# Kernel tuning notes

Measured on AMD Instinct MI355X. Metric: run time of the kernel, lower is better.

## Reference

```python
import jax, jax.numpy as jnp
import numpy as np

D_MODEL = 512
N_HEADS = 8
D_HEAD = D_MODEL // N_HEADS
SCALE = D_HEAD ** -0.5


def _rel_shift(x):
    # x: (b, h, qlen, klen) -> Transformer-XL relative shift
    b, h, qlen, klen = x.shape
    x = jnp.pad(x, ((0, 0), (0, 0), (0, 0), (1, 0)))        # (b,h,q,k+1)
    x = x.reshape(b, h, klen + 1, qlen)
    x = x[:, :, 1:, :].reshape(b, h, qlen, klen)
    return x


def setup_inputs() -> dict:
    key = jax.random.key(0)
    ks = jax.random.split(key, 12)
    B, S = 2, 2048
    P = 2 * S - 1
    w = lambda k, shape: (jax.random.normal(k, shape, jnp.float32) * 0.02)
    return {
        "x": jax.random.normal(ks[0], (B, S, D_MODEL), jnp.float32),
        "pos_emb": jax.random.normal(ks[1], (P, D_MODEL), jnp.float32),
        "Wq": w(ks[2], (D_MODEL, D_MODEL)), "bq": jnp.zeros((D_MODEL,), jnp.float32),
        "Wk": w(ks[3], (D_MODEL, D_MODEL)), "bk": jnp.zeros((D_MODEL,), jnp.float32),
        "Wv": w(ks[4], (D_MODEL, D_MODEL)), "bv": jnp.zeros((D_MODEL,), jnp.float32),
        "Wp": w(ks[5], (D_MODEL, D_MODEL)),
        "Wo": w(ks[6], (D_MODEL, D_MODEL)), "bo": jnp.zeros((D_MODEL,), jnp.float32),
        "pos_bias_u": w(ks[7], (N_HEADS, D_HEAD)),
        "pos_bias_v": w(ks[8], (N_HEADS, D_HEAD)),
    }


def reference(x, pos_emb, Wq, bq, Wk, bk, Wv, bv, Wp, Wo, bo, pos_bias_u, pos_bias_v):
    B, S, _ = x.shape
    # projections (torch Linear: y = x @ W^T + b; here W stored as (in, out))
    q = (x @ Wq + bq).reshape(B, S, N_HEADS, D_HEAD)
    k = (x @ Wk + bk).reshape(B, S, N_HEADS, D_HEAD)
    v = (x @ Wv + bv).reshape(B, S, N_HEADS, D_HEAD)
    p = (pos_emb @ Wp).reshape(-1, N_HEADS, D_HEAD)  # (2S-1, H, D)

    # content score: (q + u) @ k^T  -> (B,H,S,S)
    content = jnp.einsum("bshd,bthd->bhst", q + pos_bias_u, k)
    # position score: (q + v_bias) @ p^T -> (B,H,S,2S-1), then rel_shift
    pos = jnp.einsum("bshd,phd->bhsp", q + pos_bias_v, p)
    pos = _rel_shift(pos)[..., :S]  # trim to kv_len

    attn = jax.nn.softmax((content + pos) * SCALE, axis=-1)
    out = jnp.einsum("bhst,bthd->bshd", attn, v).reshape(B, S, D_MODEL)
    out = out @ Wo + bo
    return out
```

## Files before the change

kernel.cpp:

```cpp
#include <hip/hip_runtime.h>

#define DM    512
#define NH    8
#define DH    64
#define SEQ   2048
#define PLEN  4095
#define NB    2
#define ATT_SCALE 0.125f

typedef __attribute__((ext_vector_type(8))) _Float16 half8;
typedef __attribute__((ext_vector_type(4))) float   floatx4;

__global__ __launch_bounds__(256)
void prep(const float* __restrict__ x, const float* __restrict__ pe,
          const float* __restrict__ W0, const float* __restrict__ W1,
          const float* __restrict__ W2, const float* __restrict__ W3,
          const float* __restrict__ W4,
          _Float16* __restrict__ x16, _Float16* __restrict__ pe16,
          _Float16* __restrict__ Wt)
{
    __shared__ _Float16 tile[64 * 72];
    const int z = blockIdx.z;
    const int t = threadIdx.x;

    if (z < 2) {
        const float* src = z ? pe : x;
        _Float16* dst = z ? pe16 : x16;
        const long n = z ? (long)PLEN * DM : (long)NB * SEQ * DM;
        const long i = ((long)blockIdx.x * 256 + t) * 8;
        if (i >= n) return;
        float4 f0 = *(const float4*)(src + i);
        float4 f1 = *(const float4*)(src + i + 4);
        half8 o;
        o[0] = (_Float16)f0.x; o[1] = (_Float16)f0.y;
        o[2] = (_Float16)f0.z; o[3] = (_Float16)f0.w;
        o[4] = (_Float16)f1.x; o[5] = (_Float16)f1.y;
        o[6] = (_Float16)f1.z; o[7] = (_Float16)f1.w;
        *(half8*)(dst + i) = o;
        return;
    }
    if (blockIdx.x >= 64) return;
    const int wz = z - 2;
    const float* W = (wz == 0) ? W0 : (wz == 1) ? W1 : (wz == 2) ? W2
                   : (wz == 3) ? W3 : W4;
    _Float16* dst_base = Wt + (size_t)wz * DM * DM;
    const int n0 = (blockIdx.x & 7) * 64, k0 = (blockIdx.x >> 3) * 64;
    {
        const int kr = t >> 2, nch = (t & 3) * 16;
        const float* src = W + (size_t)(k0 + kr) * DM + n0 + nch;
        float4 f0 = *(const float4*)(src + 0);
        float4 f1 = *(const float4*)(src + 4);
        float4 f2 = *(const float4*)(src + 8);
        float4 f3 = *(const float4*)(src + 12);
        _Float16* trow = &tile[kr * 72 + nch];
        trow[0]  = (_Float16)f0.x; trow[1]  = (_Float16)f0.y;
        trow[2]  = (_Float16)f0.z; trow[3]  = (_Float16)f0.w;
        trow[4]  = (_Float16)f1.x; trow[5]  = (_Float16)f1.y;
        trow[6]  = (_Float16)f1.z; trow[7]  = (_Float16)f1.w;
        trow[8]  = (_Float16)f2.x; trow[9]  = (_Float16)f2.y;
        trow[10] = (_Float16)f2.z; trow[11] = (_Float16)f2.w;
        trow[12] = (_Float16)f3.x; trow[13] = (_Float16)f3.y;
        trow[14] = (_Float16)f3.z; trow[15] = (_Float16)f3.w;
    }
    __syncthreads();
    {
        const int nr = t >> 2, kch = (t & 3) * 16;
        half8 o0, o1;
#pragma unroll
        for (int i = 0; i < 8; ++i) o0[i] = tile[(kch + i) * 72 + nr];
#pragma unroll
        for (int i = 0; i < 8; ++i) o1[i] = tile[(kch + 8 + i) * 72 + nr];
        _Float16* dst = dst_base + (size_t)(n0 + nr) * DM + k0 + kch;
        *(half8*)dst = o0;
        *(half8*)(dst + 8) = o1;
    }
}

__global__ __launch_bounds__(256)
void gemm_qkvp(const _Float16* __restrict__ X, const _Float16* __restrict__ Pe,
               const _Float16* __restrict__ Wt,
               const float* __restrict__ bq, const float* __restrict__ bk,
               const float* __restrict__ bv, const float* __restrict__ bu,
               const float* __restrict__ bvb,
               _Float16* __restrict__ qu16, _Float16* __restrict__ qv16,
               _Float16* __restrict__ k16, _Float16* __restrict__ vt16,
               _Float16* __restrict__ p16)
{
    __shared__ _Float16 aS[64 * 72];
    __shared__ _Float16 wS[64 * 72];

    const int t = threadIdx.x;
    const int w = t >> 6, lane = t & 63, quad = lane >> 4, l16 = lane & 15;
    const int z = blockIdx.z;
    const int n0 = blockIdx.x * 64;
    const int m0 = blockIdx.y * 64;
    const int srow = t >> 2, sch = (t & 3) * 16;
    const _Float16* A = (z == 3) ? Pe : X;
    const _Float16* Wz = Wt + (size_t)z * DM * DM;

    int arow = m0 + srow;
    if (z == 3 && arow > PLEN - 1) arow = PLEN - 1;
    const _Float16* arowp = A + (size_t)arow * DM + sch;
    const _Float16* wrowp = Wz + (size_t)(n0 + srow) * DM + sch;

    floatx4 acc[4];
#pragma unroll
    for (int ct = 0; ct < 4; ++ct) acc[ct] = (floatx4){0.f, 0.f, 0.f, 0.f};

    half8 pa0 = *(const half8*)arowp;
    half8 pa1 = *(const half8*)(arowp + 8);
    half8 pw0 = *(const half8*)wrowp;
    half8 pw1 = *(const half8*)(wrowp + 8);

    for (int k0 = 0; k0 < DM; k0 += 64) {
        __syncthreads();
        *(half8*)&aS[srow * 72 + sch]     = pa0;
        *(half8*)&aS[srow * 72 + sch + 8] = pa1;
        *(half8*)&wS[srow * 72 + sch]     = pw0;
        *(half8*)&wS[srow * 72 + sch + 8] = pw1;
        __syncthreads();
        if (k0 + 64 < DM) {
            pa0 = *(const half8*)(arowp + k0 + 64);
            pa1 = *(const half8*)(arowp + k0 + 72);
            pw0 = *(const half8*)(wrowp + k0 + 64);
            pw1 = *(const half8*)(wrowp + k0 + 72);
        }
#pragma unroll
        for (int kb = 0; kb < 2; ++kb) {
            half8 af = *(const half8*)&aS[(16 * w + l16) * 72 + kb * 32 + quad * 8];
#pragma unroll
            for (int ct = 0; ct < 4; ++ct) {
                half8 bf = *(const half8*)&wS[(16 * ct + l16) * 72 + kb * 32 + quad * 8];
                acc[ct] = __builtin_amdgcn_mfma_f32_16x16x32_f16(af, bf, acc[ct], 0, 0, 0);
            }
        }
    }

    const int h = n0 >> 6;
    if (z == 0) {
#pragma unroll
        for (int ct = 0; ct < 4; ++ct) {
            const int n = n0 + 16 * ct + l16;
            const float bval = bq[n], uval = bu[n], vval = bvb[n];
#pragma unroll
            for (int r = 0; r < 4; ++r) {
                const int m = m0 + 16 * w + 4 * quad + r;
                const int b = m >> 11, s = m & 2047;
                const size_t dst = ((size_t)((h * NB + b) * SEQ) + s) * DH + (n & 63);
                const float q = acc[ct][r] + bval;
                qu16[dst] = (_Float16)((q + uval) * ATT_SCALE);
                qv16[dst] = (_Float16)((q + vval) * ATT_SCALE);
            }
        }
    } else if (z == 1) {
#pragma unroll
        for (int ct = 0; ct < 4; ++ct) {
            const int n = n0 + 16 * ct + l16;
            const float bval = bk[n];
#pragma unroll
            for (int r = 0; r < 4; ++r) {
                const int m = m0 + 16 * w + 4 * quad + r;
                const int b = m >> 11, s = m & 2047;
                k16[((size_t)((h * NB + b) * SEQ) + s) * DH + (n & 63)] =
                    (_Float16)(acc[ct][r] + bval);
            }
        }
    } else if (z == 2) {
        __syncthreads();
#pragma unroll
        for (int ct = 0; ct < 4; ++ct) {
            const float bval = bv[n0 + 16 * ct + l16];
#pragma unroll
            for (int r = 0; r < 4; ++r)
                aS[(16 * w + 4 * quad + r) * 72 + 16 * ct + l16] =
                    (_Float16)(acc[ct][r] + bval);
        }
        __syncthreads();
        const int b = m0 >> 11, s0 = m0 & 2047;
        const int drow = t >> 2;
        half8 o0, o1;
#pragma unroll
        for (int i = 0; i < 8; ++i) o0[i] = aS[(sch + i) * 72 + drow];
#pragma unroll
        for (int i = 0; i < 8; ++i) o1[i] = aS[(sch + 8 + i) * 72 + drow];
        _Float16* dst = vt16 + ((size_t)((h * NB + b) * DH) + drow) * SEQ + s0 + sch;
        *(half8*)dst = o0;
        *(half8*)(dst + 8) = o1;
    } else {
#pragma unroll
        for (int ct = 0; ct < 4; ++ct) {
            const int n = n0 + 16 * ct + l16;
#pragma unroll
            for (int r = 0; r < 4; ++r) {
                const int m = m0 + 16 * w + 4 * quad + r;
                if (m < PLEN)
                    p16[((size_t)h * PLEN + m) * DH + (n & 63)] = (_Float16)acc[ct][r];
            }
        }
    }
}

__global__ __launch_bounds__(256, 2)
void relattn_mfma(const _Float16* __restrict__ QU,
                  const _Float16* __restrict__ QV,
                  const _Float16* __restrict__ Kp,
                  const _Float16* __restrict__ VT,
                  const _Float16* __restrict__ Pp,
                  _Float16* __restrict__ Out)
{
    __shared__ _Float16 kS[64 * 72];
    __shared__ _Float16 pS[128 * 72];
    __shared__ _Float16 vS[64 * 72];
    __shared__ _Float16 tS[64 * 88];

    const int t = threadIdx.x;
    const int w = t >> 6, lane = t & 63, quad = lane >> 4, l16 = lane & 15;
    const int i0 = blockIdx.x * 64;
    const int h = blockIdx.y, b = blockIdx.z;
    const size_t hb = (size_t)(h * NB + b);
    const int cbase = 48 - 16 * w;

    half8 qa[2], va[2];
    {
        const _Float16* qrow = QU + (hb * SEQ + i0 + 16 * w + l16) * DH + quad * 8;
        const _Float16* vrow = QV + (hb * SEQ + i0 + 16 * w + l16) * DH + quad * 8;
        qa[0] = *(const half8*)qrow;       qa[1] = *(const half8*)(qrow + 32);
        va[0] = *(const half8*)vrow;       va[1] = *(const half8*)(vrow + 32);
    }

    floatx4 O[4];
    float lsum[4] = {0.f, 0.f, 0.f, 0.f};
#pragma unroll
    for (int ct = 0; ct < 4; ++ct) O[ct] = (floatx4){0.f, 0.f, 0.f, 0.f};

    const int srow = t >> 2, schunk = (t & 3) * 16;
    const int prow = t >> 1, pch = (t & 1) * 32;

    const _Float16* Kbase = Kp + hb * SEQ * DH;
    const _Float16* Vbase = VT + hb * DH * SEQ;
    const _Float16* Pbase = Pp + (size_t)h * PLEN * DH;
    const int rbase0 = (SEQ - 1) - i0 - 63;

    half8 pk0, pk1, pv0, pv1;
    half8 pp0 = {}, pp1 = {}, pp2 = {}, pp3 = {};
    {
        const _Float16* src = Kbase + (size_t)srow * DH + schunk;
        pk0 = *(const half8*)src;
        pk1 = *(const half8*)(src + 8);
        const _Float16* vsrc = Vbase + (size_t)srow * SEQ + schunk;
        pv0 = *(const half8*)vsrc;
        pv1 = *(const half8*)(vsrc + 8);
        if (prow < 127) {
            const _Float16* psrc = Pbase + (size_t)(rbase0 + prow) * DH + pch;
            pp0 = *(const half8*)(psrc + 0);
            pp1 = *(const half8*)(psrc + 8);
            pp2 = *(const half8*)(psrc + 16);
            pp3 = *(const half8*)(psrc + 24);
        }
    }

    for (int j0 = 0; j0 < SEQ; j0 += 64) {
        __syncthreads();

        *(half8*)&kS[srow * 72 + schunk]     = pk0;
        *(half8*)&kS[srow * 72 + schunk + 8] = pk1;
        *(half8*)&vS[srow * 72 + schunk]     = pv0;
        *(half8*)&vS[srow * 72 + schunk + 8] = pv1;
        if (prow < 127) {
            *(half8*)&pS[prow * 72 + pch + 0]  = pp0;
            *(half8*)&pS[prow * 72 + pch + 8]  = pp1;
            *(half8*)&pS[prow * 72 + pch + 16] = pp2;
            *(half8*)&pS[prow * 72 + pch + 24] = pp3;
        }
        __syncthreads();

        if (j0 + 64 < SEQ) {
            const _Float16* src = Kbase + (size_t)(j0 + 64 + srow) * DH + schunk;
            pk0 = *(const half8*)src;
            pk1 = *(const half8*)(src + 8);
            const _Float16* vsrc = Vbase + (size_t)srow * SEQ + j0 + 64 + schunk;
            pv0 = *(const half8*)vsrc;
            pv1 = *(const half8*)(vsrc + 8);
            if (prow < 127) {
                const _Float16* psrc = Pbase + (size_t)(rbase0 + j0 + 64 + prow) * DH + pch;
                pp0 = *(const half8*)(psrc + 0);
                pp1 = *(const half8*)(psrc + 8);
                pp2 = *(const half8*)(psrc + 16);
                pp3 = *(const half8*)(psrc + 24);
            }
        }

        {
            floatx4 Tacc[5];
#pragma unroll
            for (int c2 = 0; c2 < 5; ++c2) Tacc[c2] = (floatx4){0.f, 0.f, 0.f, 0.f};
#pragma unroll
            for (int kb = 0; kb < 2; ++kb) {
#pragma unroll
                for (int c2 = 0; c2 < 5; ++c2) {
                    half8 bf = *(const half8*)&pS[(cbase + 16 * c2 + l16) * 72 + kb * 32 + quad * 8];
                    Tacc[c2] = __builtin_amdgcn_mfma_f32_16x16x32_f16(va[kb], bf, Tacc[c2], 0, 0, 0);
                }
            }
#pragma unroll
            for (int c2 = 0; c2 < 5; ++c2)
#pragma unroll
                for (int r = 0; r < 4; ++r)
                    tS[(16 * w + 4 * quad + r) * 88 + 16 * c2 + l16] = (_Float16)Tacc[c2][r];
        }
        asm volatile("" ::: "memory");

        floatx4 Sc[4];
#pragma unroll
        for (int ct = 0; ct < 4; ++ct) Sc[ct] = (floatx4){0.f, 0.f, 0.f, 0.f};
#pragma unroll
        for (int kb = 0; kb < 2; ++kb) {
#pragma unroll
            for (int ct = 0; ct < 4; ++ct) {
                half8 bf = *(const half8*)&kS[(16 * ct + l16) * 72 + kb * 32 + quad * 8];
                Sc[ct] = __builtin_amdgcn_mfma_f32_16x16x32_f16(qa[kb], bf, Sc[ct], 0, 0, 0);
            }
        }
#pragma unroll
        for (int ct = 0; ct < 4; ++ct)
#pragma unroll
            for (int r = 0; r < 4; ++r) {
                const int il16 = 4 * quad + r;
                const int c = 16 * ct + l16 - il16 + 15;
                const float e = __expf(Sc[ct][r] +
                                       (float)tS[(16 * w + il16) * 88 + c]);
                Sc[ct][r] = e;
                lsum[r] += e;
            }
        asm volatile("" ::: "memory");

#pragma unroll
        for (int ct = 0; ct < 4; ++ct)
#pragma unroll
            for (int r = 0; r < 4; ++r)
                tS[(16 * w + 4 * quad + r) * 88 + 16 * ct + l16] = (_Float16)Sc[ct][r];
        asm volatile("" ::: "memory");

#pragma unroll
        for (int kb = 0; kb < 2; ++kb) {
            half8 af = *(const half8*)&tS[(16 * w + l16) * 88 + kb * 32 + quad * 8];
#pragma unroll
            for (int ct = 0; ct < 4; ++ct) {
                half8 bf = *(const half8*)&vS[(16 * ct + l16) * 72 + kb * 32 + quad * 8];
                O[ct] = __builtin_amdgcn_mfma_f32_16x16x32_f16(af, bf, O[ct], 0, 0, 0);
            }
        }
        asm volatile("" ::: "memory");
    }

#pragma unroll
    for (int r = 0; r < 4; ++r) {
#pragma unroll
        for (int m = 1; m < 16; m <<= 1) lsum[r] += __shfl_xor(lsum[r], m);
        const float inv = 1.f / lsum[r];
        _Float16* orow = Out + (size_t)(b * SEQ + i0 + 16 * w + 4 * quad + r) * DM + h * DH;
#pragma unroll
        for (int ct = 0; ct < 4; ++ct)
            orow[16 * ct + l16] = (_Float16)(O[ct][r] * inv);
    }
}

__global__ __launch_bounds__(256)
void gemm_out(const _Float16* __restrict__ A, const _Float16* __restrict__ Wt,
              const float* __restrict__ bias, float* __restrict__ Out)
{
    __shared__ _Float16 aS[64 * 72];
    __shared__ _Float16 wS[64 * 72];

    const int t = threadIdx.x;
    const int w = t >> 6, lane = t & 63, quad = lane >> 4, l16 = lane & 15;
    const int n0 = blockIdx.x * 64;
    const int m0 = blockIdx.y * 64;
    const int srow = t >> 2, sch = (t & 3) * 16;

    const _Float16* arowp = A + (size_t)(m0 + srow) * DM + sch;
    const _Float16* wrowp = Wt + (size_t)(n0 + srow) * DM + sch;

    floatx4 acc[4];
#pragma unroll
    for (int ct = 0; ct < 4; ++ct) acc[ct] = (floatx4){0.f, 0.f, 0.f, 0.f};

    half8 pa0 = *(const half8*)arowp;
    half8 pa1 = *(const half8*)(arowp + 8);
    half8 pw0 = *(const half8*)wrowp;
    half8 pw1 = *(const half8*)(wrowp + 8);

    for (int k0 = 0; k0 < DM; k0 += 64) {
        __syncthreads();
        *(half8*)&aS[srow * 72 + sch]     = pa0;
        *(half8*)&aS[srow * 72 + sch + 8] = pa1;
        *(half8*)&wS[srow * 72 + sch]     = pw0;
        *(half8*)&wS[srow * 72 + sch + 8] = pw1;
        __syncthreads();
        if (k0 + 64 < DM) {
            pa0 = *(const half8*)(arowp + k0 + 64);
            pa1 = *(const half8*)(arowp + k0 + 72);
            pw0 = *(const half8*)(wrowp + k0 + 64);
            pw1 = *(const half8*)(wrowp + k0 + 72);
        }
#pragma unroll
        for (int kb = 0; kb < 2; ++kb) {
            half8 af = *(const half8*)&aS[(16 * w + l16) * 72 + kb * 32 + quad * 8];
#pragma unroll
            for (int ct = 0; ct < 4; ++ct) {
                half8 bf = *(const half8*)&wS[(16 * ct + l16) * 72 + kb * 32 + quad * 8];
                acc[ct] = __builtin_amdgcn_mfma_f32_16x16x32_f16(af, bf, acc[ct], 0, 0, 0);
            }
        }
    }

#pragma unroll
    for (int ct = 0; ct < 4; ++ct) {
        const int n = n0 + 16 * ct + l16;
        const float bval = bias[n];
#pragma unroll
        for (int r = 0; r < 4; ++r) {
            const int m = m0 + 16 * w + 4 * quad + r;
            Out[(size_t)m * DM + n] = acc[ct][r] + bval;
        }
    }
}

extern "C" void kernel_launch(void* const* d_in, const int* in_sizes, int n_in,
                              void* d_out, int out_size, void* d_ws, size_t ws_size,
                              hipStream_t stream)
{
    (void)in_sizes; (void)n_in; (void)out_size; (void)ws_size;
    const float* x   = (const float*)d_in[0];
    const float* pe  = (const float*)d_in[1];
    const float* Wq  = (const float*)d_in[2];
    const float* bq  = (const float*)d_in[3];
    const float* Wk  = (const float*)d_in[4];
    const float* bk  = (const float*)d_in[5];
    const float* Wv  = (const float*)d_in[6];
    const float* bv  = (const float*)d_in[7];
    const float* Wp  = (const float*)d_in[8];
    const float* Wo  = (const float*)d_in[9];
    const float* bo  = (const float*)d_in[10];
    const float* pbu = (const float*)d_in[11];
    const float* pbv = (const float*)d_in[12];
    float* out = (float*)d_out;

    const size_t nX  = (size_t)NB * SEQ * DM;
    const size_t nPe = (size_t)PLEN * DM;
    const size_t nW  = (size_t)DM * DM;
    const size_t nH  = (size_t)NH * NB * SEQ * DH;
    const size_t nPh = (size_t)NH * PLEN * DH;

    _Float16* x16  = (_Float16*)d_ws;
    _Float16* pe16 = x16 + nX;
    _Float16* wt   = pe16 + nPe;
    _Float16* qu16 = wt + 5 * nW;
    _Float16* qv16 = qu16 + nH;
    _Float16* k16  = qv16 + nH;
    _Float16* vt16 = k16 + nH;
    _Float16* p16  = vt16 + nH;
    _Float16* ow16 = p16 + nPh;

    dim3 blk(256);
    prep<<<dim3(1024, 1, 7), blk, 0, stream>>>(x, pe, Wq, Wk, Wv, Wp, Wo,
                                               x16, pe16, wt);
    gemm_qkvp<<<dim3(8, 64, 4), blk, 0, stream>>>(x16, pe16, wt,
                                                  bq, bk, bv, pbu, pbv,
                                                  qu16, qv16, k16, vt16, p16);
    relattn_mfma<<<dim3(SEQ / 64, NH, NB), blk, 0, stream>>>(
        qu16, qv16, k16, vt16, p16, ow16);
    gemm_out<<<dim3(8, 64), blk, 0, stream>>>(ow16, wt + 4 * nW, bo, out);
}
```

Baseline: 187.3 us.

## Split attention over key halves, async LDS double-buffering, bpermute rel-shift

Measured after the change: 200.9 us. +7.2%, slower.

```diff
diff --git a/kernel.cpp b/kernel.cpp
--- a/kernel.cpp
+++ b/kernel.cpp
@@ -10,6 +10,12 @@
 
 typedef __attribute__((ext_vector_type(8))) _Float16 half8;
 typedef __attribute__((ext_vector_type(4))) float   floatx4;
+
+__device__ __forceinline__ void gll16(const _Float16* g, _Float16* l) {
+    __builtin_amdgcn_global_load_lds(
+        (const __attribute__((address_space(1))) void*)g,
+        (__attribute__((address_space(3))) void*)l, 16, 0, 0);
+}
 
 __global__ __launch_bounds__(256)
 void prep(const float* __restrict__ x, const float* __restrict__ pe,
@@ -206,19 +212,20 @@
                   const _Float16* __restrict__ Kp,
                   const _Float16* __restrict__ VT,
                   const _Float16* __restrict__ Pp,
-                  _Float16* __restrict__ Out)
+                  float* __restrict__ Opart,
+                  float* __restrict__ Lpart)
 {
-    __shared__ _Float16 kS[64 * 72];
-    __shared__ _Float16 pS[128 * 72];
-    __shared__ _Float16 vS[64 * 72];
-    __shared__ _Float16 tS[64 * 88];
+    __shared__ _Float16 sbuf[2][16384];
+    __shared__ _Float16 tS[64 * 72];
 
     const int t = threadIdx.x;
     const int w = t >> 6, lane = t & 63, quad = lane >> 4, l16 = lane & 15;
     const int i0 = blockIdx.x * 64;
-    const int h = blockIdx.y, b = blockIdx.z;
+    const int h = blockIdx.y;
+    const int b = blockIdx.z & 1, jh = blockIdx.z >> 1;
     const size_t hb = (size_t)(h * NB + b);
     const int cbase = 48 - 16 * w;
+    const int jbeg = jh * (SEQ / 2), jend = jbeg + (SEQ / 2);
 
     half8 qa[2], va[2];
     {
@@ -233,140 +240,143 @@
 #pragma unroll
     for (int ct = 0; ct < 4; ++ct) O[ct] = (floatx4){0.f, 0.f, 0.f, 0.f};
 
-    const int srow = t >> 2, schunk = (t & 3) * 16;
-    const int prow = t >> 1, pch = (t & 1) * 32;
-
     const _Float16* Kbase = Kp + hb * SEQ * DH;
     const _Float16* Vbase = VT + hb * DH * SEQ;
     const _Float16* Pbase = Pp + (size_t)h * PLEN * DH;
     const int rbase0 = (SEQ - 1) - i0 - 63;
 
-    half8 pk0, pk1, pv0, pv1;
-    half8 pp0 = {}, pp1 = {}, pp2 = {}, pp3 = {};
-    {
-        const _Float16* src = Kbase + (size_t)srow * DH + schunk;
-        pk0 = *(const half8*)src;
-        pk1 = *(const half8*)(src + 8);
-        const _Float16* vsrc = Vbase + (size_t)srow * SEQ + schunk;
-        pv0 = *(const half8*)vsrc;
-        pv1 = *(const half8*)(vsrc + 8);
-        if (prow < 127) {
-            const _Float16* psrc = Pbase + (size_t)(rbase0 + prow) * DH + pch;
-            pp0 = *(const half8*)(psrc + 0);
-            pp1 = *(const half8*)(psrc + 8);
-            pp2 = *(const half8*)(psrc + 16);
-            pp3 = *(const half8*)(psrc + 24);
-        }
-    }
-
-    for (int j0 = 0; j0 < SEQ; j0 += 64) {
-        __syncthreads();
-
-        *(half8*)&kS[srow * 72 + schunk]     = pk0;
-        *(half8*)&kS[srow * 72 + schunk + 8] = pk1;
-        *(half8*)&vS[srow * 72 + schunk]     = pv0;
-        *(half8*)&vS[srow * 72 + schunk + 8] = pv1;
-        if (prow < 127) {
-            *(half8*)&pS[prow * 72 + pch + 0]  = pp0;
-            *(half8*)&pS[prow * 72 + pch + 8]  = pp1;
-            *(half8*)&pS[prow * 72 + pch + 16] = pp2;
-            *(half8*)&pS[prow * 72 + pch + 24] = pp3;
-        }
-        __syncthreads();
-
-        if (j0 + 64 < SEQ) {
-            const _Float16* src = Kbase + (size_t)(j0 + 64 + srow) * DH + schunk;
-            pk0 = *(const half8*)src;
-            pk1 = *(const half8*)(src + 8);
-            const _Float16* vsrc = Vbase + (size_t)srow * SEQ + j0 + 64 + schunk;
-            pv0 = *(const half8*)vsrc;
-            pv1 = *(const half8*)(vsrc + 8);
-            if (prow < 127) {
-                const _Float16* psrc = Pbase + (size_t)(rbase0 + j0 + 64 + prow) * DH + pch;
-                pp0 = *(const half8*)(psrc + 0);
-                pp1 = *(const half8*)(psrc + 8);
-                pp2 = *(const half8*)(psrc + 16);
-                pp3 = *(const half8*)(psrc + 24);
-            }
-        }
-
-        {
-            floatx4 Tacc[5];
-#pragma unroll
-            for (int c2 = 0; c2 < 5; ++c2) Tacc[c2] = (floatx4){0.f, 0.f, 0.f, 0.f};
-#pragma unroll
-            for (int kb = 0; kb < 2; ++kb) {
-#pragma unroll
-                for (int c2 = 0; c2 < 5; ++c2) {
-                    half8 bf = *(const half8*)&pS[(cbase + 16 * c2 + l16) * 72 + kb * 32 + quad * 8];
-                    Tacc[c2] = __builtin_amdgcn_mfma_f32_16x16x32_f16(va[kb], bf, Tacc[c2], 0, 0, 0);
-                }
-            }
+    const int kx = l16 & 7;
+    const int hox0 = ((quad) ^ kx) * 8;
+    const int hox1 = ((4 + quad) ^ kx) * 8;
+
+    const int l3 = lane >> 3, pos = lane & 7;
+
+#define STAGE(bufp, J0)                                                        \
+    {                                                                          \
+        _Float16* bp = (bufp);                                                 \
+        const int rb = rbase0 + (J0);                                          \
+        _Pragma("unroll")                                                      \
+        for (int I = 0; I < 2; ++I) {                                          \
+            const int cid = w * 2 + I;                                         \
+            const int row = cid * 8 + l3;                                      \
+            const int ch  = pos ^ (row & 7);                                   \
+            gll16(Kbase + (size_t)((J0) + row) * DH + ch * 8, bp + cid * 512); \
+        }                                                                      \
+        _Pragma("unroll")                                                      \
+        for (int I = 0; I < 2; ++I) {                                          \
+            const int cid = w * 2 + I;                                         \
+            const int row = cid * 8 + l3;                                      \
+            const int ch  = pos ^ (row & 7);                                   \
+            gll16(Vbase + (size_t)row * SEQ + (J0) + ch * 8,                   \
+                  bp + 4096 + cid * 512);                                      \
+        }                                                                      \
+        _Pragma("unroll")                                                      \
+        for (int I = 0; I < 4; ++I) {                                          \
+            const int cid = w * 4 + I;                                         \
+            const int row = cid * 8 + l3;                                      \
+            int r = rb + row; if (r > PLEN - 1) r = PLEN - 1;                  \
+            const int ch  = pos ^ (row & 7);                                   \
+            gll16(Pbase + (size_t)r * DH + ch * 8, bp + 8192 + cid * 512);     \
+        }                                                                      \
+    }
+
+    STAGE(&sbuf[0][0], jbeg);
+
+    int cur = 0;
+    for (int j0 = jbeg; j0 < jend; j0 += 64) {
+        asm volatile("s_waitcnt vmcnt(0)" ::: "memory");
+        __builtin_amdgcn_s_barrier();
+        asm volatile("" ::: "memory");
+
+        const _Float16* kSc = &sbuf[cur][0];
+        const _Float16* vSc = &sbuf[cur][4096];
+        const _Float16* pSc = &sbuf[cur][8192];
+
+        if (j0 + 64 < jend) STAGE(&sbuf[cur ^ 1][0], j0 + 64);
+
+        floatx4 Tacc[5];
+#pragma unroll
+        for (int c2 = 0; c2 < 5; ++c2) Tacc[c2] = (floatx4){0.f, 0.f, 0.f, 0.f};
+#pragma unroll
+        for (int c2 = 0; c2 < 5; ++c2) {
+            half8 bf0 = *(const half8*)&pSc[(cbase + 16 * c2 + l16) * 64 + hox0];
+            half8 bf1 = *(const half8*)&pSc[(cbase + 16 * c2 + l16) * 64 + hox1];
+            Tacc[c2] = __builtin_amdgcn_mfma_f32_16x16x32_f16(va[0], bf0, Tacc[c2], 0, 0, 0);
+            Tacc[c2] = __builtin_amdgcn_mfma_f32_16x16x32_f16(va[1], bf1, Tacc[c2], 0, 0, 0);
+        }
+
+        floatx4 Sc[4];
+#pragma unroll
+        for (int ct = 0; ct < 4; ++ct) Sc[ct] = (floatx4){0.f, 0.f, 0.f, 0.f};
+#pragma unroll
+        for (int ct = 0; ct < 4; ++ct) {
+            half8 bf0 = *(const half8*)&kSc[(16 * ct + l16) * 64 + hox0];
+            half8 bf1 = *(const half8*)&kSc[(16 * ct + l16) * 64 + hox1];
+            Sc[ct] = __builtin_amdgcn_mfma_f32_16x16x32_f16(qa[0], bf0, Sc[ct], 0, 0, 0);
+            Sc[ct] = __builtin_amdgcn_mfma_f32_16x16x32_f16(qa[1], bf1, Sc[ct], 0, 0, 0);
+        }
+
+#pragma unroll
+        for (int r = 0; r < 4; ++r) {
+            const int u  = l16 - 4 * quad - r + 15;
+            const int dl = u & 15;
+            const int s  = u >> 4;
+            const int pidx = (((quad << 4) | dl) << 2);
+            float rot[5];
 #pragma unroll
             for (int c2 = 0; c2 < 5; ++c2)
-#pragma unroll
-                for (int r = 0; r < 4; ++r)
-                    tS[(16 * w + 4 * quad + r) * 88 + 16 * c2 + l16] = (_Float16)Tacc[c2][r];
-        }
-        asm volatile("" ::: "memory");
-
-        floatx4 Sc[4];
-#pragma unroll
-        for (int ct = 0; ct < 4; ++ct) Sc[ct] = (floatx4){0.f, 0.f, 0.f, 0.f};
-#pragma unroll
-        for (int kb = 0; kb < 2; ++kb) {
+                rot[c2] = __int_as_float(__builtin_amdgcn_ds_bpermute(
+                    pidx, __float_as_int(Tacc[c2][r])));
 #pragma unroll
             for (int ct = 0; ct < 4; ++ct) {
-                half8 bf = *(const half8*)&kS[(16 * ct + l16) * 72 + kb * 32 + quad * 8];
-                Sc[ct] = __builtin_amdgcn_mfma_f32_16x16x32_f16(qa[kb], bf, Sc[ct], 0, 0, 0);
-            }
-        }
-#pragma unroll
-        for (int ct = 0; ct < 4; ++ct)
-#pragma unroll
-            for (int r = 0; r < 4; ++r) {
-                const int il16 = 4 * quad + r;
-                const int c = 16 * ct + l16 - il16 + 15;
-                const float e = __expf(Sc[ct][r] +
-                                       (float)tS[(16 * w + il16) * 88 + c]);
+                const float tv = s ? rot[ct + 1] : rot[ct];
+                const float e = __expf(Sc[ct][r] + tv);
                 Sc[ct][r] = e;
                 lsum[r] += e;
             }
+        }
+
+#pragma unroll
+        for (int ct = 0; ct < 4; ++ct)
+#pragma unroll
+            for (int r = 0; r < 4; ++r)
+                tS[(16 * w + 4 * quad + r) * 72 + 16 * ct + l16] = (_Float16)Sc[ct][r];
         asm volatile("" ::: "memory");
 
 #pragma unroll
+        for (int kb = 0; kb < 2; ++kb) {
+            half8 af = *(const half8*)&tS[(16 * w + l16) * 72 + kb * 32 + quad * 8];
+            const int hox = kb ? hox1 : hox0;
+#pragma unroll
+            for (int ct = 0; ct < 4; ++ct) {
+                half8 bf = *(const half8*)&vSc[(16 * ct + l16) * 64 + hox];
+                O[ct] = __builtin_amdgcn_mfma_f32_16x16x32_f16(af, bf, O[ct], 0, 0, 0);
+            }
+        }
+        asm volatile("" ::: "memory");
+        cur ^= 1;
+    }
+#undef STAGE
+
+    float* Op = Opart + (size_t)jh * NB * SEQ * DM;
+    float* Lp = Lpart + (size_t)jh * NH * NB * SEQ;
+#pragma unroll
+    for (int r = 0; r < 4; ++r) {
+#pragma unroll
+        for (int m = 1; m < 16; m <<= 1) lsum[r] += __shfl_xor(lsum[r], m);
+        const int row = i0 + 16 * w + 4 * quad + r;
+        if (l16 == 0) Lp[hb * SEQ + row] = lsum[r];
+        float* orow = Op + (size_t)(b * SEQ + row) * DM + h * DH;
+#pragma unroll
         for (int ct = 0; ct < 4; ++ct)
-#pragma unroll
-            for (int r = 0; r < 4; ++r)
-                tS[(16 * w + 4 * quad + r) * 88 + 16 * ct + l16] = (_Float16)Sc[ct][r];
-        asm volatile("" ::: "memory");
-
-#pragma unroll
-        for (int kb = 0; kb < 2; ++kb) {
-            half8 af = *(const half8*)&tS[(16 * w + l16) * 88 + kb * 32 + quad * 8];
-#pragma unroll
-            for (int ct = 0; ct < 4; ++ct) {
-                half8 bf = *(const half8*)&vS[(16 * ct + l16) * 72 + kb * 32 + quad * 8];
-                O[ct] = __builtin_amdgcn_mfma_f32_16x16x32_f16(af, bf, O[ct], 0, 0, 0);
-            }
-        }
-        asm volatile("" ::: "memory");
-    }
-
-#pragma unroll
-    for (int r = 0; r < 4; ++r) {
-#pragma unroll
-        for (int m = 1; m < 16; m <<= 1) lsum[r] += __shfl_xor(lsum[r], m);
-        const float inv = 1.f / lsum[r];
-        _Float16* orow = Out + (size_t)(b * SEQ + i0 + 16 * w + 4 * quad + r) * DM + h * DH;
-#pragma unroll
-        for (int ct = 0; ct < 4; ++ct)
-            orow[16 * ct + l16] = (_Float16)(O[ct][r] * inv);
+            orow[16 * ct + l16] = O[ct][r];
     }
 }
 
 __global__ __launch_bounds__(256)
-void gemm_out(const _Float16* __restrict__ A, const _Float16* __restrict__ Wt,
+void gemm_out(const float* __restrict__ O0, const float* __restrict__ O1,
+              const float* __restrict__ L0, const float* __restrict__ L1,
+              const _Float16* __restrict__ Wt,
               const float* __restrict__ bias, float* __restrict__ Out)
 {
     __shared__ _Float16 aS[64 * 72];
@@ -378,28 +388,63 @@
     const int m0 = blockIdx.y * 64;
     const int srow = t >> 2, sch = (t & 3) * 16;
 
-    const _Float16* arowp = A + (size_t)(m0 + srow) * DM + sch;
+    const int mrow = m0 + srow;
+    const int bA = mrow >> 11, sA = mrow & 2047;
+    const float* o0p = O0 + (size_t)mrow * DM + sch;
+    const float* o1p = O1 + (size_t)mrow * DM + sch;
     const _Float16* wrowp = Wt + (size_t)(n0 + srow) * DM + sch;
 
     floatx4 acc[4];
 #pragma unroll
     for (int ct = 0; ct < 4; ++ct) acc[ct] = (floatx4){0.f, 0.f, 0.f, 0.f};
 
-    half8 pa0 = *(const half8*)arowp;
-    half8 pa1 = *(const half8*)(arowp + 8);
+    float4 pa0 = *(const float4*)(o0p + 0);
+    float4 pa1 = *(const float4*)(o0p + 4);
+    float4 pa2 = *(const float4*)(o0p + 8);
+    float4 pa3 = *(const float4*)(o0p + 12);
+    float4 pc0 = *(const float4*)(o1p + 0);
+    float4 pc1 = *(const float4*)(o1p + 4);
+    float4 pc2 = *(const float4*)(o1p + 8);
+    float4 pc3 = *(const float4*)(o1p + 12);
     half8 pw0 = *(const half8*)wrowp;
     half8 pw1 = *(const half8*)(wrowp + 8);
 
     for (int k0 = 0; k0 < DM; k0 += 64) {
         __syncthreads();
-        *(half8*)&aS[srow * 72 + sch]     = pa0;
-        *(half8*)&aS[srow * 72 + sch + 8] = pa1;
+        const int hA = k0 >> 6;
+        const int li = (hA * NB + bA) * SEQ + sA;
+        const float inv = 1.f / (L0[li] + L1[li]);
+        half8 h0, h1;
+        h0[0] = (_Float16)((pa0.x + pc0.x) * inv);
+        h0[1] = (_Float16)((pa0.y + pc0.y) * inv);
+        h0[2] = (_Float16)((pa0.z + pc0.z) * inv);
+        h0[3] = (_Float16)((pa0.w + pc0.w) * inv);
+        h0[4] = (_Float16)((pa1.x + pc1.x) * inv);
+        h0[5] = (_Float16)((pa1.y + pc1.y) * inv);
+        h0[6] = (_Float16)((pa1.z + pc1.z) * inv);
+        h0[7] = (_Float16)((pa1.w + pc1.w) * inv);
+        h1[0] = (_Float16)((pa2.x + pc2.x) * inv);
+        h1[1] = (_Float16)((pa2.y + pc2.y) * inv);
+        h1[2] = (_Float16)((pa2.z + pc2.z) * inv);
+        h1[3] = (_Float16)((pa2.w + pc2.w) * inv);
+        h1[4] = (_Float16)((pa3.x + pc3.x) * inv);
+        h1[5] = (_Float16)((pa3.y + pc3.y) * inv);
+        h1[6] = (_Float16)((pa3.z + pc3.z) * inv);
+        h1[7] = (_Float16)((pa3.w + pc3.w) * inv);
+        *(half8*)&aS[srow * 72 + sch]     = h0;
+        *(half8*)&aS[srow * 72 + sch + 8] = h1;
         *(half8*)&wS[srow * 72 + sch]     = pw0;
         *(half8*)&wS[srow * 72 + sch + 8] = pw1;
         __syncthreads();
         if (k0 + 64 < DM) {
-            pa0 = *(const half8*)(arowp + k0 + 64);
-            pa1 = *(const half8*)(arowp + k0 + 72);
+            pa0 = *(const float4*)(o0p + k0 + 64);
+            pa1 = *(const float4*)(o0p + k0 + 68);
+            pa2 = *(const float4*)(o0p + k0 + 72);
+            pa3 = *(const float4*)(o0p + k0 + 76);
+            pc0 = *(const float4*)(o1p + k0 + 64);
+            pc1 = *(const float4*)(o1p + k0 + 68);
+            pc2 = *(const float4*)(o1p + k0 + 72);
+            pc3 = *(const float4*)(o1p + k0 + 76);
             pw0 = *(const half8*)(wrowp + k0 + 64);
             pw1 = *(const half8*)(wrowp + k0 + 72);
         }
@@ -451,6 +496,7 @@
     const size_t nW  = (size_t)DM * DM;
     const size_t nH  = (size_t)NH * NB * SEQ * DH;
     const size_t nPh = (size_t)NH * PLEN * DH;
+    const size_t nL  = (size_t)NH * NB * SEQ;
 
     _Float16* x16  = (_Float16*)d_ws;
     _Float16* pe16 = x16 + nX;
@@ -461,6 +507,8 @@
     _Float16* vt16 = k16 + nH;
     _Float16* p16  = vt16 + nH;
     _Float16* ow16 = p16 + nPh;
+    float*    opart = (float*)(ow16 + nX);
+    float*    lpart = opart + 2 * nX;
 
     dim3 blk(256);
     prep<<<dim3(1024, 1, 7), blk, 0, stream>>>(x, pe, Wq, Wk, Wv, Wp, Wo,
@@ -468,7 +516,9 @@
     gemm_qkvp<<<dim3(8, 64, 4), blk, 0, stream>>>(x16, pe16, wt,
                                                   bq, bk, bv, pbu, pbv,
                                                   qu16, qv16, k16, vt16, p16);
-    relattn_mfma<<<dim3(SEQ / 64, NH, NB), blk, 0, stream>>>(
-        qu16, qv16, k16, vt16, p16, ow16);
-    gemm_out<<<dim3(8, 64), blk, 0, stream>>>(ow16, wt + 4 * nW, bo, out);
+    relattn_mfma<<<dim3(SEQ / 64, NH, NB * 2), blk, 0, stream>>>(
+        qu16, qv16, k16, vt16, p16, opart, lpart);
+    gemm_out<<<dim3(8, 64), blk, 0, stream>>>(opart, opart + nX,
+                                              lpart, lpart + nL,
+                                              wt + 4 * nW, bo, out);
 }
```
